# Kernel optimization log

Hardware: AMD Instinct MI355X
Metric: run time of the kernel (lower is better)

The kernel has to match this reference:

```python
import jax, jax.numpy as jnp
import numpy as np

ROPE_BASE = 10000.0

def apply_rope(x):
    # x: (BS, T, H, hd). 1D RoPE over temporal axis with rotate-half convention.
    BS, T, H, hd = x.shape
    half = hd // 2
    inv_freq = 1.0 / (ROPE_BASE ** (jnp.arange(0, half, dtype=jnp.float32) / half))
    angles = jnp.arange(T, dtype=jnp.float32)[:, None] * inv_freq[None, :]  # (T, half)
    cos = jnp.concatenate([jnp.cos(angles), jnp.cos(angles)], axis=-1)[None, :, None, :]  # (1,T,1,hd)
    sin = jnp.concatenate([jnp.sin(angles), jnp.sin(angles)], axis=-1)[None, :, None, :]
    x1, x2 = x[..., :half], x[..., half:]
    x_rot = jnp.concatenate([-x2, x1], axis=-1)
    return (x * cos + x_rot * sin).astype(x.dtype)

def setup_inputs() -> dict:
    key = jax.random.key(0)
    ks = jax.random.split(key, 7)
    B, T_p, T_f, S, d = 4, 8, 8, 256, 512
    v_p = jax.random.normal(ks[0], (B, T_p, S, d), dtype=jnp.float32)
    v_f = jax.random.normal(ks[1], (B, T_f, S, d), dtype=jnp.float32)
    a_p = jax.random.normal(ks[2], (B, T_p, d), dtype=jnp.float32)
    a_f = jax.random.normal(ks[3], (B, T_f, d), dtype=jnp.float32)
    W_qkv = jax.random.normal(ks[4], (d, 3 * d), dtype=jnp.float32) * (d ** -0.5)
    W_proj = jax.random.normal(ks[5], (d, d), dtype=jnp.float32) * (d ** -0.5)
    b_proj = jnp.zeros((d,), dtype=jnp.float32)
    return {"v_p": v_p, "v_f": v_f, "a_p": a_p, "a_f": a_f,
            "W_qkv": W_qkv, "W_proj": W_proj, "b_proj": b_proj}

def reference(v_p, v_f, a_p, a_f, W_qkv, W_proj, b_proj):
    num_heads = 8
    B, T_p, S, d = v_p.shape
    T_f = v_f.shape[1]
    hd = d // num_heads
    scale = hd ** -0.5

    # rearrange 'b t s d -> (b s) t d'
    vp = jnp.transpose(v_p, (0, 2, 1, 3)).reshape(B * S, T_p, d)
    vf = jnp.transpose(v_f, (0, 2, 1, 3)).reshape(B * S, T_f, d)
    # repeat 'b t d -> (b s) t d'
    ap = jnp.broadcast_to(a_p[:, None], (B, S, T_p, d)).reshape(B * S, T_p, d)
    af = jnp.broadcast_to(a_f[:, None], (B, S, T_f, d)).reshape(B * S, T_f, d)

    tokens = jnp.concatenate([vp, vf, ap, af], axis=1)  # (BS, total_T, d)
    BS, total_T = tokens.shape[0], tokens.shape[1]

    qkv = tokens @ W_qkv  # (BS, total_T, 3d), no bias
    q, k, v = jnp.split(qkv, 3, axis=-1)
    q = q.reshape(BS, total_T, num_heads, hd)
    k = k.reshape(BS, total_T, num_heads, hd)
    v = v.reshape(BS, total_T, num_heads, hd)

    q = apply_rope(q)
    k = apply_rope(k)

    # joint bidirectional attention over total_T
    attn = jnp.einsum('bthd,bThd->bhtT', q, k) * scale
    attn = jax.nn.softmax(attn, axis=-1)
    out = jnp.einsum('bhtT,bThd->bthd', attn, v).reshape(BS, total_T, d)

    out = out @ W_proj + b_proj

    vp_o = out[:, :T_p]
    vf_o = out[:, T_p:T_p + T_f]
    ap_o = out[:, T_p + T_f:T_p + T_f + T_p]
    af_o = out[:, T_p + T_f + T_p:]

    # '(b s) t d -> b t s d'
    vp_o = jnp.transpose(vp_o.reshape(B, S, T_p, d), (0, 2, 1, 3))
    vf_o = jnp.transpose(vf_o.reshape(B, S, T_f, d), (0, 2, 1, 3))
    # '(b s) t d -> b s t d' then mean over s
    ap_o = ap_o.reshape(B, S, T_p, d).mean(axis=1)
    af_o = af_o.reshape(B, S, T_f, d).mean(axis=1)
    return (vp_o, vf_o, ap_o, af_o)
```

## Files before the change

### kernel.cpp

```cpp
#include <hip/hip_runtime.h>
#include <math.h>

#define BB   4
#define SS   256
#define DD   512
#define HH   8
#define HD   64
#define HALF 32
#define TT   32
#define TV   16
#define W3   1536
#define MROWS  16448
#define MPAD   16512

#define VP_BASE 0
#define VF_BASE 4194304
#define AP_BASE 8388608
#define AF_BASE 8404992

#define LN10000_OVER_HALF (9.210340371976184f / 32.0f)

typedef _Float16 h2 __attribute__((ext_vector_type(2)));
typedef _Float16 h4 __attribute__((ext_vector_type(4)));
typedef _Float16 h8 __attribute__((ext_vector_type(8)));
typedef float    f4 __attribute__((ext_vector_type(4)));
typedef float    f16v __attribute__((ext_vector_type(16)));

__device__ __forceinline__ float ropefreq(int i) {
    return __expf(-(float)i * LN10000_OVER_HALF);
}

typedef __attribute__((address_space(3))) void*       lds_ptr_t;
typedef const __attribute__((address_space(1))) void* gbl_ptr_t;
__device__ __forceinline__ void async16(const void* g, void* l) {
    __builtin_amdgcn_global_load_lds((gbl_ptr_t)g, (lds_ptr_t)l, 16, 0, 0);
}

__device__ __forceinline__ int xcd_swz(int bid, int nwg) {
    int q = nwg >> 3, r = nwg & 7;
    int xcd = bid & 7, off = bid >> 3;
    return (xcd < r ? xcd * (q + 1) : r * (q + 1) + (xcd - r) * q) + off;
}

__global__ __launch_bounds__(256)
void conv_kernel(const float* __restrict__ v_p, const float* __restrict__ v_f,
                 const float* __restrict__ a_p, const float* __restrict__ a_f,
                 const float* __restrict__ Wqkv, const float* __restrict__ Wp,
                 _Float16* __restrict__ tok, _Float16* __restrict__ Wt,
                 _Float16* __restrict__ Wpt, float2* __restrict__ rope) {
    __shared__ float tile[64 * 65];
    const int bid = blockIdx.x, tid = threadIdx.x;
    if (bid < 8224) {
        int id = bid * 256 + tid;
        int e  = id * 4;
        int r  = e >> 9, c = e & 511;
        const float* src;
        if (r < 16384) {
            int bs = r >> 4, t = r & 15, b = bs >> 8, s = bs & 255;
            src = (t < 8) ? v_p + (size_t)((b * 8 + t) * SS + s) * DD
                          : v_f + (size_t)((b * 8 + t - 8) * SS + s) * DD;
        } else {
            int idx = r - 16384, b = idx >> 4, t2 = idx & 15;
            src = (t2 < 8) ? a_p + (size_t)(b * 8 + t2) * DD
                           : a_f + (size_t)(b * 8 + (t2 - 8)) * DD;
        }
        float4 v = *(const float4*)(src + c);
        h4 o = { (_Float16)v.x, (_Float16)v.y, (_Float16)v.z, (_Float16)v.w };
        *(h4*)(tok + (size_t)r * DD + c) = o;
    } else if (bid < 8480) {
        int tb = bid - 8224;
        const float* src; _Float16* dst; int ld, k0, n0;
        if (tb < 192) {
            src = Wqkv; dst = Wt; ld = W3;
            k0 = (tb & 7) * 64; n0 = (tb >> 3) * 64;
        } else {
            int t2 = tb - 192;
            src = Wp; dst = Wpt; ld = DD;
            k0 = (t2 & 7) * 64; n0 = (t2 >> 3) * 64;
        }
#pragma unroll
        for (int p = 0; p < 16; ++p) {
            int idx = p * 256 + tid, rr = idx >> 6, cc = idx & 63;
            tile[rr * 65 + cc] = src[(size_t)(k0 + rr) * ld + n0 + cc];
        }
        __syncthreads();
#pragma unroll
        for (int p = 0; p < 16; ++p) {
            int idx = p * 256 + tid, rr = idx >> 6, cc = idx & 63;
            dst[(size_t)(n0 + rr) * DD + k0 + cc] = (_Float16)tile[cc * 65 + rr];
        }
    } else {
        int idx = tid * 4;
#pragma unroll
        for (int e2 = 0; e2 < 4; ++e2) {
            int ii = (idx + e2) & 31, tt = (idx + e2) >> 5;
            float ang = (float)tt * ropefreq(ii);
            float sn, cs;
            __sincosf(ang, &sn, &cs);
            rope[idx + e2] = make_float2(cs, sn);
        }
    }
}

__global__ __launch_bounds__(256, 3)
void gemm_qkv_kernel(const _Float16* __restrict__ A, const _Float16* __restrict__ Bt,
                     _Float16* __restrict__ C) {
    __shared__ __align__(16) _Float16 As[128 * 64];
    __shared__ __align__(16) _Float16 Bs[128 * 64];
    const int tid = threadIdx.x, lane = tid & 63, wave = tid >> 6;
    const int bid = xcd_swz(blockIdx.x, 129 * 12);
    const int tm = bid / 12, tn = bid % 12;
    const int m_base = (wave >> 1) * 64, n_base = (wave & 1) * 64;
    const int quad = lane >> 4, l16 = lane & 15;

    f4 acc[4][4] = {};

    int srow[4], soff[4];
#pragma unroll
    for (int p = 0; p < 4; ++p) {
        int ci = p * 256 + tid;
        int r = ci >> 3, sl = ci & 7;
        srow[p] = r;
        soff[p] = (sl ^ (r & 7)) * 8;
    }

    for (int k0 = 0; k0 < 512; k0 += 64) {
#pragma unroll
        for (int p = 0; p < 4; ++p) {
            int ci = p * 256 + tid;
            async16(A  + (size_t)(tm * 128 + srow[p]) * 512 + k0 + soff[p],
                    &As[ci * 8]);
            async16(Bt + (size_t)(tn * 128 + srow[p]) * 512 + k0 + soff[p],
                    &Bs[ci * 8]);
        }
        __syncthreads();

#pragma unroll
        for (int kk = 0; kk < 2; ++kk) {
            h8 af[4], bf[4];
#pragma unroll
            for (int mi = 0; mi < 4; ++mi) {
                int m = m_base + mi * 16 + l16;
                int sl = (kk * 4 + quad) ^ (m & 7);
                af[mi] = *(const h8*)&As[m * 64 + sl * 8];
            }
#pragma unroll
            for (int ni = 0; ni < 4; ++ni) {
                int n = n_base + ni * 16 + l16;
                int sl = (kk * 4 + quad) ^ (n & 7);
                bf[ni] = *(const h8*)&Bs[n * 64 + sl * 8];
            }
#pragma unroll
            for (int mi = 0; mi < 4; ++mi)
#pragma unroll
                for (int ni = 0; ni < 4; ++ni)
                    acc[mi][ni] = __builtin_amdgcn_mfma_f32_16x16x32_f16(
                        af[mi], bf[ni], acc[mi][ni], 0, 0, 0);
        }
        __syncthreads();
    }

#pragma unroll
    for (int mi = 0; mi < 4; ++mi)
#pragma unroll
        for (int ni = 0; ni < 4; ++ni) {
            int row = tm * 128 + m_base + mi * 16 + quad * 4;
            int col = tn * 128 + n_base + ni * 16 + l16;
#pragma unroll
            for (int r = 0; r < 4; ++r)
                C[(size_t)(row + r) * W3 + col] = (_Float16)acc[mi][ni][r];
        }
}

__global__ __launch_bounds__(256)
void attn5_kernel(const _Float16* __restrict__ qkv, const float2* __restrict__ rope,
                  _Float16* __restrict__ attnv, _Float16* __restrict__ attna) {
    __shared__ _Float16 VlA[4][32 * 72];
    __shared__ _Float16 PlA[4][32 * 40];
    const int bid = blockIdx.x;
    const int bs = bid >> 1, hh = bid & 1, b = bs >> 8, s = bs & 255;
    const int tid = threadIdx.x, wave = tid >> 6, lane = tid & 63;
    const int t = lane & 31, half = lane >> 5;
    _Float16* vl = &VlA[wave][0];
    _Float16* pl = &PlA[wave][0];
    const int h = wave + 4 * hh;

    const size_t row = (t < 16) ? (size_t)(bs * 16 + t)
                                : (size_t)(16384 + b * 16 + (t - 16));
    const _Float16* qp = qkv + row * W3 + h * HD;

    float ccA[8], ssA[8], ccB[8], ssB[8];
    const float2* rt = rope + t * 32 + 8 * half;
#pragma unroll
    for (int j = 0; j < 8; ++j) {
        float2 eA = rt[j];
        float2 eB = rt[16 + j];
        ccA[j] = eA.x; ssA[j] = eA.y;
        ccB[j] = eB.x; ssB[j] = eB.y;
    }

    h8 v0 = *(const h8*)(qp + 2 * DD + 32 * half);
    h8 v1 = *(const h8*)(qp + 2 * DD + 32 * half + 8);
    h8 v2 = *(const h8*)(qp + 2 * DD + 32 * half + 16);
    h8 v3 = *(const h8*)(qp + 2 * DD + 32 * half + 24);
    *(h8*)&vl[t * 72 + 32 * half +  0] = v0;
    *(h8*)&vl[t * 72 + 32 * half +  8] = v1;
    *(h8*)&vl[t * 72 + 32 * half + 16] = v2;
    *(h8*)&vl[t * 72 + 32 * half + 24] = v3;

    h8 q0 = *(const h8*)(qp + 8 * half);
    h8 q1 = *(const h8*)(qp + 8 * half + 16);
    h8 q2 = *(const h8*)(qp + 8 * half + 32);
    h8 q3 = *(const h8*)(qp + 8 * half + 48);
    h8 k0 = *(const h8*)(qp + DD + 8 * half);
    h8 k1 = *(const h8*)(qp + DD + 8 * half + 16);
    h8 k2 = *(const h8*)(qp + DD + 8 * half + 32);
    h8 k3 = *(const h8*)(qp + DD + 8 * half + 48);

    h8 qf0, qf1, qf2, qf3, kf0, kf1, kf2, kf3;
#pragma unroll
    for (int j = 0; j < 8; ++j) {
        float x1 = (float)q0[j], x2 = (float)q2[j];
        qf0[j] = (_Float16)(0.125f * (x1 * ccA[j] - x2 * ssA[j]));
        qf2[j] = (_Float16)(0.125f * (x2 * ccA[j] + x1 * ssA[j]));
        x1 = (float)q1[j]; x2 = (float)q3[j];
        qf1[j] = (_Float16)(0.125f * (x1 * ccB[j] - x2 * ssB[j]));
        qf3[j] = (_Float16)(0.125f * (x2 * ccB[j] + x1 * ssB[j]));
        x1 = (float)k0[j]; x2 = (float)k2[j];
        kf0[j] = (_Float16)(x1 * ccA[j] - x2 * ssA[j]);
        kf2[j] = (_Float16)(x2 * ccA[j] + x1 * ssA[j]);
        x1 = (float)k1[j]; x2 = (float)k3[j];
        kf1[j] = (_Float16)(x1 * ccB[j] - x2 * ssB[j]);
        kf3[j] = (_Float16)(x2 * ccB[j] + x1 * ssB[j]);
    }

    f16v s4 = {};
    s4 = __builtin_amdgcn_mfma_f32_32x32x16_f16(qf0, kf0, s4, 0, 0, 0);
    s4 = __builtin_amdgcn_mfma_f32_32x32x16_f16(qf1, kf1, s4, 0, 0, 0);
    s4 = __builtin_amdgcn_mfma_f32_32x32x16_f16(qf2, kf2, s4, 0, 0, 0);
    s4 = __builtin_amdgcn_mfma_f32_32x32x16_f16(qf3, kf3, s4, 0, 0, 0);

#pragma unroll
    for (int r = 0; r < 16; ++r) {
        float e = __expf(s4[r]);
        float sm = e;
#pragma unroll
        for (int mask = 1; mask <= 16; mask <<= 1)
            sm += __shfl_xor(sm, mask);
        float p = e * __builtin_amdgcn_rcpf(sm);
        int rr = (r & 3) + 8 * (r >> 2) + 4 * half;
        pl[rr * 40 + t] = (_Float16)p;
    }

    f16v o_acc[2];
#pragma unroll
    for (int n0 = 0; n0 < 2; ++n0) {
        f16v o = {};
#pragma unroll
        for (int kk = 0; kk < 2; ++kk) {
            h8 pf = *(const h8*)&pl[t * 40 + kk * 16 + half * 8];
            h8 vf;
#pragma unroll
            for (int jj = 0; jj < 8; ++jj)
                vf[jj] = vl[(kk * 16 + half * 8 + jj) * 72 + n0 * 32 + t];
            o = __builtin_amdgcn_mfma_f32_32x32x16_f16(pf, vf, o, 0, 0, 0);
        }
        o_acc[n0] = o;
    }

#pragma unroll
    for (int n0 = 0; n0 < 2; ++n0)
#pragma unroll
        for (int r = 0; r < 16; ++r) {
            int i = (r & 3) + 8 * (r >> 2) + 4 * half;
            vl[i * 72 + n0 * 32 + t] = (_Float16)o_acc[n0][r];
        }

#pragma unroll
    for (int rr = 0; rr < 4; ++rr) {
        int i = rr * 8 + (lane >> 3);
        int c = (lane & 7) * 8;
        h8 val = *(const h8*)&vl[i * 72 + c];
        if (rr < 2)
            *(h8*)&attnv[(size_t)(bs * 16 + i) * DD + h * HD + c] = val;
        else
            *(h8*)&attna[(((size_t)b * 16 + (i - 16)) * SS + s) * DD + h * HD + c] = val;
    }
}

__global__ __launch_bounds__(256)
void reduce_a_kernel(const _Float16* __restrict__ attna, _Float16* __restrict__ abar) {
    __shared__ float red[16][128];
    const int bid = blockIdx.x;
    const int r = bid >> 2, cq = bid & 3;
    const int tid = threadIdx.x;
    const int rg = tid >> 4, ch = tid & 15;

    float acc[8] = {};
    const _Float16* base = attna + ((size_t)r * SS + rg * 16) * DD + cq * 128 + ch * 8;
#pragma unroll 4
    for (int i = 0; i < 16; ++i) {
        h8 v = *(const h8*)(base + (size_t)i * DD);
#pragma unroll
        for (int j = 0; j < 8; ++j) acc[j] += (float)v[j];
    }
#pragma unroll
    for (int j = 0; j < 8; ++j) red[rg][ch * 8 + j] = acc[j];
    __syncthreads();

    if (tid < 64) {
        int c = tid * 2;
        float s0 = 0.f, s1 = 0.f;
#pragma unroll
        for (int g = 0; g < 16; ++g) { s0 += red[g][c]; s1 += red[g][c + 1]; }
        h2 o = { (_Float16)(s0 * (1.0f / SS)), (_Float16)(s1 * (1.0f / SS)) };
        *(h2*)&abar[(size_t)r * DD + cq * 128 + c] = o;
    }
}

__global__ __launch_bounds__(256, 3)
void proj_kernel(const _Float16* __restrict__ A, const _Float16* __restrict__ Bt,
                 const float* __restrict__ bp, float* __restrict__ out) {
    __shared__ __align__(16) _Float16 As[128 * 64];
    __shared__ __align__(16) _Float16 Bs[128 * 64];
    const int tid = threadIdx.x, lane = tid & 63, wave = tid >> 6;
    const int bid = xcd_swz(blockIdx.x, 129 * 4);
    const int tm = bid >> 2, tn = bid & 3;
    const int m_base = (wave >> 1) * 64, n_base = (wave & 1) * 64;
    const int quad = lane >> 4, l16 = lane & 15;

    f4 acc[4][4] = {};

    int srow[4], soff[4];
#pragma unroll
    for (int p = 0; p < 4; ++p) {
        int ci = p * 256 + tid;
        int r = ci >> 3, sl = ci & 7;
        srow[p] = r;
        soff[p] = (sl ^ (r & 7)) * 8;
    }

    for (int k0 = 0; k0 < 512; k0 += 64) {
#pragma unroll
        for (int p = 0; p < 4; ++p) {
            int ci = p * 256 + tid;
            async16(A  + (size_t)(tm * 128 + srow[p]) * 512 + k0 + soff[p],
                    &As[ci * 8]);
            async16(Bt + (size_t)(tn * 128 + srow[p]) * 512 + k0 + soff[p],
                    &Bs[ci * 8]);
        }
        __syncthreads();

#pragma unroll
        for (int kk = 0; kk < 2; ++kk) {
            h8 af[4], bf[4];
#pragma unroll
            for (int mi = 0; mi < 4; ++mi) {
                int m = m_base + mi * 16 + l16;
                int sl = (kk * 4 + quad) ^ (m & 7);
                af[mi] = *(const h8*)&As[m * 64 + sl * 8];
            }
#pragma unroll
            for (int ni = 0; ni < 4; ++ni) {
                int n = n_base + ni * 16 + l16;
                int sl = (kk * 4 + quad) ^ (n & 7);
                bf[ni] = *(const h8*)&Bs[n * 64 + sl * 8];
            }
#pragma unroll
            for (int mi = 0; mi < 4; ++mi)
#pragma unroll
                for (int ni = 0; ni < 4; ++ni)
                    acc[mi][ni] = __builtin_amdgcn_mfma_f32_16x16x32_f16(
                        af[mi], bf[ni], acc[mi][ni], 0, 0, 0);
        }
        __syncthreads();
    }

#pragma unroll
    for (int mi = 0; mi < 4; ++mi)
#pragma unroll
        for (int ni = 0; ni < 4; ++ni) {
            int row0 = tm * 128 + m_base + mi * 16 + quad * 4;
            int col  = tn * 128 + n_base + ni * 16 + l16;
            float bias = bp[col];
#pragma unroll
            for (int r = 0; r < 4; ++r) {
                int row = row0 + r;
                float val = acc[mi][ni][r] + bias;
                if (row < 16384) {
                    int bsq = row >> 4, t = row & 15;
                    int b = bsq >> 8, s = bsq & 255;
                    size_t off = (t < 8)
                        ? (VP_BASE + (size_t)((b * 8 + t) * SS + s) * DD + col)
                        : (VF_BASE + (size_t)((b * 8 + t - 8) * SS + s) * DD + col);
                    out[off] = val;
                } else if (row < 16448) {
                    int idx = row - 16384;
                    int b = idx >> 4, t2 = idx & 15;
                    size_t off = (t2 < 8)
                        ? (AP_BASE + (size_t)(b * 8 + t2) * DD + col)
                        : (AF_BASE + (size_t)(b * 8 + (t2 - 8)) * DD + col);
                    out[off] = val;
                }
            }
        }
}

extern "C" void kernel_launch(void* const* d_in, const int* in_sizes, int n_in,
                              void* d_out, int out_size, void* d_ws, size_t ws_size,
                              hipStream_t stream) {
    const float* v_p  = (const float*)d_in[0];
    const float* v_f  = (const float*)d_in[1];
    const float* a_p  = (const float*)d_in[2];
    const float* a_f  = (const float*)d_in[3];
    const float* Wqkv = (const float*)d_in[4];
    const float* Wp   = (const float*)d_in[5];
    const float* bp   = (const float*)d_in[6];
    float* out = (float*)d_out;

    char* w = (char*)d_ws;
    _Float16* tok   = (_Float16*)w;  w += (size_t)MPAD * DD * 2;
    _Float16* qkv   = (_Float16*)w;  w += (size_t)MPAD * W3 * 2;
    _Float16* attnv = (_Float16*)w;  w += (size_t)MPAD * DD * 2;
    _Float16* Wt    = (_Float16*)w;  w += (size_t)W3 * DD * 2;
    _Float16* Wpt   = (_Float16*)w;  w += (size_t)DD * DD * 2;
    float2*   rope  = (float2*)w;    w += (size_t)1024 * sizeof(float2);
    _Float16* attna = tok;
    _Float16* abar  = attnv + (size_t)16384 * DD;

    conv_kernel<<<8481, 256, 0, stream>>>(v_p, v_f, a_p, a_f, Wqkv, Wp,
                                          tok, Wt, Wpt, rope);
    gemm_qkv_kernel<<<129 * 12, 256, 0, stream>>>(tok, Wt, qkv);
    attn5_kernel<<<2048, 256, 0, stream>>>(qkv, rope, attnv, attna);
    reduce_a_kernel<<<256, 256, 0, stream>>>(attna, abar);
    proj_kernel<<<129 * 4, 256, 0, stream>>>(attnv, Wpt, bp, out);
}
```

Baseline: 174.6 us.

## Fuse fp32-to-fp16 token gather/conversion into QKV GEMM A-tile loads

Removes the token gather/convert pass from the prep kernel. The QKV GEMM now reads the fp32 activations directly, converts them to fp16 and stores them to LDS with synchronous loads instead of async global-to-LDS copies. This saves writing and re-reading a 16 MB fp16 token buffer, but each activation is read in fp32 by all 12 N-tiles. The A loads are no longer asynchronous, which may stall the GEMM.

New measurement: 186.3 us. 6.7% more time.

```diff
diff --git a/kernel.cpp b/kernel.cpp
--- a/kernel.cpp
+++ b/kernel.cpp
@@ -43,32 +43,13 @@
 }
 
 __global__ __launch_bounds__(256)
-void conv_kernel(const float* __restrict__ v_p, const float* __restrict__ v_f,
-                 const float* __restrict__ a_p, const float* __restrict__ a_f,
-                 const float* __restrict__ Wqkv, const float* __restrict__ Wp,
-                 _Float16* __restrict__ tok, _Float16* __restrict__ Wt,
-                 _Float16* __restrict__ Wpt, float2* __restrict__ rope) {
+void conv_kernel(const float* __restrict__ Wqkv, const float* __restrict__ Wp,
+                 _Float16* __restrict__ Wt, _Float16* __restrict__ Wpt,
+                 float2* __restrict__ rope) {
     __shared__ float tile[64 * 65];
     const int bid = blockIdx.x, tid = threadIdx.x;
-    if (bid < 8224) {
-        int id = bid * 256 + tid;
-        int e  = id * 4;
-        int r  = e >> 9, c = e & 511;
-        const float* src;
-        if (r < 16384) {
-            int bs = r >> 4, t = r & 15, b = bs >> 8, s = bs & 255;
-            src = (t < 8) ? v_p + (size_t)((b * 8 + t) * SS + s) * DD
-                          : v_f + (size_t)((b * 8 + t - 8) * SS + s) * DD;
-        } else {
-            int idx = r - 16384, b = idx >> 4, t2 = idx & 15;
-            src = (t2 < 8) ? a_p + (size_t)(b * 8 + t2) * DD
-                           : a_f + (size_t)(b * 8 + (t2 - 8)) * DD;
-        }
-        float4 v = *(const float4*)(src + c);
-        h4 o = { (_Float16)v.x, (_Float16)v.y, (_Float16)v.z, (_Float16)v.w };
-        *(h4*)(tok + (size_t)r * DD + c) = o;
-    } else if (bid < 8480) {
-        int tb = bid - 8224;
+    if (bid < 256) {
+        int tb = bid;
         const float* src; _Float16* dst; int ld, k0, n0;
         if (tb < 192) {
             src = Wqkv; dst = Wt; ld = W3;
@@ -103,8 +84,9 @@
 }
 
 __global__ __launch_bounds__(256, 3)
-void gemm_qkv_kernel(const _Float16* __restrict__ A, const _Float16* __restrict__ Bt,
-                     _Float16* __restrict__ C) {
+void gemm_qkv_kernel(const float* __restrict__ v_p, const float* __restrict__ v_f,
+                     const float* __restrict__ a_p, const float* __restrict__ a_f,
+                     const _Float16* __restrict__ Bt, _Float16* __restrict__ C) {
     __shared__ __align__(16) _Float16 As[128 * 64];
     __shared__ __align__(16) _Float16 Bs[128 * 64];
     const int tid = threadIdx.x, lane = tid & 63, wave = tid >> 6;
@@ -116,20 +98,43 @@
     f4 acc[4][4] = {};
 
     int srow[4], soff[4];
+    const float* srcA[4];
 #pragma unroll
     for (int p = 0; p < 4; ++p) {
         int ci = p * 256 + tid;
         int r = ci >> 3, sl = ci & 7;
         srow[p] = r;
         soff[p] = (sl ^ (r & 7)) * 8;
+        int rg = tm * 128 + r;
+        const float* s;
+        if (rg < 16384) {
+            int bs = rg >> 4, t = rg & 15, b = bs >> 8, ss = bs & 255;
+            s = (t < 8) ? v_p + (size_t)((b * 8 + t) * SS + ss) * DD
+                        : v_f + (size_t)((b * 8 + t - 8) * SS + ss) * DD;
+        } else if (rg < 16448) {
+            int idx = rg - 16384, b = idx >> 4, t2 = idx & 15;
+            s = (t2 < 8) ? a_p + (size_t)(b * 8 + t2) * DD
+                         : a_f + (size_t)(b * 8 + (t2 - 8)) * DD;
+        } else {
+            s = a_p;
+        }
+        srcA[p] = s;
     }
 
     for (int k0 = 0; k0 < 512; k0 += 64) {
 #pragma unroll
         for (int p = 0; p < 4; ++p) {
             int ci = p * 256 + tid;
-            async16(A  + (size_t)(tm * 128 + srow[p]) * 512 + k0 + soff[p],
-                    &As[ci * 8]);
+            const float* sp = srcA[p] + k0 + soff[p];
+            float4 w0 = *(const float4*)(sp);
+            float4 w1 = *(const float4*)(sp + 4);
+            h8 o = { (_Float16)w0.x, (_Float16)w0.y, (_Float16)w0.z, (_Float16)w0.w,
+                     (_Float16)w1.x, (_Float16)w1.y, (_Float16)w1.z, (_Float16)w1.w };
+            *(h8*)&As[ci * 8] = o;
+        }
+#pragma unroll
+        for (int p = 0; p < 4; ++p) {
+            int ci = p * 256 + tid;
             async16(Bt + (size_t)(tn * 128 + srow[p]) * 512 + k0 + soff[p],
                     &Bs[ci * 8]);
         }
@@ -419,18 +424,16 @@
     float* out = (float*)d_out;
 
     char* w = (char*)d_ws;
-    _Float16* tok   = (_Float16*)w;  w += (size_t)MPAD * DD * 2;
+    _Float16* attna = (_Float16*)w;  w += (size_t)MPAD * DD * 2;
     _Float16* qkv   = (_Float16*)w;  w += (size_t)MPAD * W3 * 2;
     _Float16* attnv = (_Float16*)w;  w += (size_t)MPAD * DD * 2;
     _Float16* Wt    = (_Float16*)w;  w += (size_t)W3 * DD * 2;
     _Float16* Wpt   = (_Float16*)w;  w += (size_t)DD * DD * 2;
     float2*   rope  = (float2*)w;    w += (size_t)1024 * sizeof(float2);
-    _Float16* attna = tok;
     _Float16* abar  = attnv + (size_t)16384 * DD;
 
-    conv_kernel<<<8481, 256, 0, stream>>>(v_p, v_f, a_p, a_f, Wqkv, Wp,
-                                          tok, Wt, Wpt, rope);
-    gemm_qkv_kernel<<<129 * 12, 256, 0, stream>>>(tok, Wt, qkv);
+    conv_kernel<<<257, 256, 0, stream>>>(Wqkv, Wp, Wt, Wpt, rope);
+    gemm_qkv_kernel<<<129 * 12, 256, 0, stream>>>(v_p, v_f, a_p, a_f, Wt, qkv);
     attn5_kernel<<<2048, 256, 0, stream>>>(qkv, rope, attnv, attna);
     reduce_a_kernel<<<256, 256, 0, stream>>>(attna, abar);
     proj_kernel<<<129 * 4, 256, 0, stream>>>(attnv, Wpt, bp, out);
```

## Double-buffer LDS tiles in QKV and projection GEMMs to overlap loads

Applied to the files above, without the earlier changes.

Both GEMM kernels now keep two LDS buffers per operand. The async global-to-LDS copy of the next K tile is issued before computing on the current tile, which removes one barrier per iteration and hides load latency behind MFMA work. LDS per block doubles to 64KB, so the launch-bounds occupancy hint drops from 3 to 2 blocks per CU. There is a correctness risk: the single barrier per iteration must also cover completion of the async copies, which depends on how async16 and the wait counts are handled.

Measured after the change: 194.3 us. 11.3% more time.

```diff
diff --git a/kernel.cpp b/kernel.cpp
--- a/kernel.cpp
+++ b/kernel.cpp
@@ -102,11 +102,11 @@
     }
 }
 
-__global__ __launch_bounds__(256, 3)
+__global__ __launch_bounds__(256, 2)
 void gemm_qkv_kernel(const _Float16* __restrict__ A, const _Float16* __restrict__ Bt,
                      _Float16* __restrict__ C) {
-    __shared__ __align__(16) _Float16 As[128 * 64];
-    __shared__ __align__(16) _Float16 Bs[128 * 64];
+    __shared__ __align__(16) _Float16 As[2][128 * 64];
+    __shared__ __align__(16) _Float16 Bs[2][128 * 64];
     const int tid = threadIdx.x, lane = tid & 63, wave = tid >> 6;
     const int bid = xcd_swz(blockIdx.x, 129 * 12);
     const int tm = bid / 12, tn = bid % 12;
@@ -124,17 +124,29 @@
         soff[p] = (sl ^ (r & 7)) * 8;
     }
 
-    for (int k0 = 0; k0 < 512; k0 += 64) {
-#pragma unroll
-        for (int p = 0; p < 4; ++p) {
-            int ci = p * 256 + tid;
-            async16(A  + (size_t)(tm * 128 + srow[p]) * 512 + k0 + soff[p],
-                    &As[ci * 8]);
-            async16(Bt + (size_t)(tn * 128 + srow[p]) * 512 + k0 + soff[p],
-                    &Bs[ci * 8]);
-        }
-        __syncthreads();
-
+    const _Float16* Ab = A  + (size_t)(tm * 128) * 512;
+    const _Float16* Bb = Bt + (size_t)(tn * 128) * 512;
+
+#pragma unroll
+    for (int p = 0; p < 4; ++p) {
+        int ci = p * 256 + tid;
+        async16(Ab + (size_t)srow[p] * 512 + soff[p], &As[0][ci * 8]);
+        async16(Bb + (size_t)srow[p] * 512 + soff[p], &Bs[0][ci * 8]);
+    }
+    __syncthreads();
+
+    int cur = 0;
+    for (int t = 0; t < 8; ++t) {
+        if (t < 7) {
+            int k0 = (t + 1) * 64;
+            int nxt = cur ^ 1;
+#pragma unroll
+            for (int p = 0; p < 4; ++p) {
+                int ci = p * 256 + tid;
+                async16(Ab + (size_t)srow[p] * 512 + k0 + soff[p], &As[nxt][ci * 8]);
+                async16(Bb + (size_t)srow[p] * 512 + k0 + soff[p], &Bs[nxt][ci * 8]);
+            }
+        }
 #pragma unroll
         for (int kk = 0; kk < 2; ++kk) {
             h8 af[4], bf[4];
@@ -142,13 +154,13 @@
             for (int mi = 0; mi < 4; ++mi) {
                 int m = m_base + mi * 16 + l16;
                 int sl = (kk * 4 + quad) ^ (m & 7);
-                af[mi] = *(const h8*)&As[m * 64 + sl * 8];
+                af[mi] = *(const h8*)&As[cur][m * 64 + sl * 8];
             }
 #pragma unroll
             for (int ni = 0; ni < 4; ++ni) {
                 int n = n_base + ni * 16 + l16;
                 int sl = (kk * 4 + quad) ^ (n & 7);
-                bf[ni] = *(const h8*)&Bs[n * 64 + sl * 8];
+                bf[ni] = *(const h8*)&Bs[cur][n * 64 + sl * 8];
             }
 #pragma unroll
             for (int mi = 0; mi < 4; ++mi)
@@ -157,7 +169,8 @@
                     acc[mi][ni] = __builtin_amdgcn_mfma_f32_16x16x32_f16(
                         af[mi], bf[ni], acc[mi][ni], 0, 0, 0);
         }
-        __syncthreads();
+        if (t < 7) __syncthreads();
+        cur ^= 1;
     }
 
 #pragma unroll
@@ -318,11 +331,11 @@
     }
 }
 
-__global__ __launch_bounds__(256, 3)
+__global__ __launch_bounds__(256, 2)
 void proj_kernel(const _Float16* __restrict__ A, const _Float16* __restrict__ Bt,
                  const float* __restrict__ bp, float* __restrict__ out) {
-    __shared__ __align__(16) _Float16 As[128 * 64];
-    __shared__ __align__(16) _Float16 Bs[128 * 64];
+    __shared__ __align__(16) _Float16 As[2][128 * 64];
+    __shared__ __align__(16) _Float16 Bs[2][128 * 64];
     const int tid = threadIdx.x, lane = tid & 63, wave = tid >> 6;
     const int bid = xcd_swz(blockIdx.x, 129 * 4);
     const int tm = bid >> 2, tn = bid & 3;
@@ -340,17 +353,29 @@
         soff[p] = (sl ^ (r & 7)) * 8;
     }
 
-    for (int k0 = 0; k0 < 512; k0 += 64) {
-#pragma unroll
-        for (int p = 0; p < 4; ++p) {
-            int ci = p * 256 + tid;
-            async16(A  + (size_t)(tm * 128 + srow[p]) * 512 + k0 + soff[p],
-                    &As[ci * 8]);
-            async16(Bt + (size_t)(tn * 128 + srow[p]) * 512 + k0 + soff[p],
-                    &Bs[ci * 8]);
-        }
-        __syncthreads();
-
+    const _Float16* Ab = A  + (size_t)(tm * 128) * 512;
+    const _Float16* Bb = Bt + (size_t)(tn * 128) * 512;
+
+#pragma unroll
+    for (int p = 0; p < 4; ++p) {
+        int ci = p * 256 + tid;
+        async16(Ab + (size_t)srow[p] * 512 + soff[p], &As[0][ci * 8]);
+        async16(Bb + (size_t)srow[p] * 512 + soff[p], &Bs[0][ci * 8]);
+    }
+    __syncthreads();
+
+    int cur = 0;
+    for (int t = 0; t < 8; ++t) {
+        if (t < 7) {
+            int k0 = (t + 1) * 64;
+            int nxt = cur ^ 1;
+#pragma unroll
+            for (int p = 0; p < 4; ++p) {
+                int ci = p * 256 + tid;
+                async16(Ab + (size_t)srow[p] * 512 + k0 + soff[p], &As[nxt][ci * 8]);
+                async16(Bb + (size_t)srow[p] * 512 + k0 + soff[p], &Bs[nxt][ci * 8]);
+            }
+        }
 #pragma unroll
         for (int kk = 0; kk < 2; ++kk) {
             h8 af[4], bf[4];
@@ -358,13 +383,13 @@
             for (int mi = 0; mi < 4; ++mi) {
                 int m = m_base + mi * 16 + l16;
                 int sl = (kk * 4 + quad) ^ (m & 7);
-                af[mi] = *(const h8*)&As[m * 64 + sl * 8];
+                af[mi] = *(const h8*)&As[cur][m * 64 + sl * 8];
             }
 #pragma unroll
             for (int ni = 0; ni < 4; ++ni) {
                 int n = n_base + ni * 16 + l16;
                 int sl = (kk * 4 + quad) ^ (n & 7);
-                bf[ni] = *(const h8*)&Bs[n * 64 + sl * 8];
+                bf[ni] = *(const h8*)&Bs[cur][n * 64 + sl * 8];
             }
 #pragma unroll
             for (int mi = 0; mi < 4; ++mi)
@@ -373,7 +398,8 @@
                     acc[mi][ni] = __builtin_amdgcn_mfma_f32_16x16x32_f16(
                         af[mi], bf[ni], acc[mi][ni], 0, 0, 0);
         }
-        __syncthreads();
+        if (t < 7) __syncthreads();
+        cur ^= 1;
     }
 
 #pragma unroll
```
